# Performance work log

Measured on AMD Instinct MI355X. Metric: run time of the kernel, lower is better.

Reference implementation:

```python
import jax, jax.numpy as jnp
import numpy as np

N_NODES = 50000
N_EDGES = 800000
D = 64  # in_dim = hidden_dim = out_dim


def gcn_conv(x, edge_index, W, b, num_nodes):
    """PyG GCNConv: x' = D^{-1/2} (A + I) D^{-1/2} (x W) + b."""
    h = x @ W  # [N, out]
    # add self-loops
    loop = jnp.arange(num_nodes, dtype=edge_index.dtype)
    row = jnp.concatenate([edge_index[0], loop])  # sources j
    col = jnp.concatenate([edge_index[1], loop])  # targets i
    # symmetric normalization
    ones = jnp.ones(row.shape[0], dtype=h.dtype)
    deg = jax.ops.segment_sum(ones, col, num_segments=num_nodes)
    dinv = jnp.where(deg > 0, jax.lax.rsqrt(deg), 0.0)
    norm = dinv[row] * dinv[col]  # [E+N]
    # gather -> scale -> scatter-add
    msg = h[row] * norm[:, None]
    out = jax.ops.segment_sum(msg, col, num_segments=num_nodes)
    return out + b


def setup_inputs() -> dict:
    key = jax.random.key(0)
    k = jax.random.split(key, 6)
    x = jax.random.normal(k[0], (N_NODES, D), dtype=jnp.float32)
    edge_index = jax.random.randint(k[1], (2, N_EDGES), 0, N_NODES, dtype=jnp.int64)
    s = 1.0 / np.sqrt(D)
    W1 = jax.random.uniform(k[2], (D, D), jnp.float32, -s, s)
    b1 = jnp.zeros((D,), jnp.float32)
    W2 = jax.random.uniform(k[3], (D, D), jnp.float32, -s, s)
    b2 = jnp.zeros((D,), jnp.float32)
    return {"x": x, "edge_index": edge_index, "W1": W1, "b1": b1, "W2": W2, "b2": b2}


def reference(x, edge_index, W1, b1, W2, b2):
    h = gcn_conv(x, edge_index, W1, b1, N_NODES)
    h = jax.nn.relu(h)
    out = gcn_conv(h, edge_index, W2, b2, N_NODES)
    return out
```

## Files before the change

### kernel.cpp

```cpp
#include <hip/hip_runtime.h>
#include <hip/hip_fp16.h>

#define N_NODES 50000
#define N_EDGES 800000
#define D 64
#define RANGES 8
#define SLICES 16
#define NPB (N_NODES / RANGES)
#define I4S (N_EDGES / SLICES / 4)
#define CAP 48
#define PFX_BLOCKS (N_NODES / 4)
#define GEMM_BLOCKS (N_NODES / 16)

__global__ __launch_bounds__(1024)
void count_kernel(const int* __restrict__ col, unsigned char* __restrict__ cnt8) {
    __shared__ int cur[NPB];
    int tid = threadIdx.x;
    int r = blockIdx.x & (RANGES - 1), s = blockIdx.x >> 3;
    int lo = r * NPB;
    for (int i = tid; i < NPB; i += 1024) cur[i] = 0;
    __syncthreads();
    const int4* c4 = (const int4*)col;
    for (int i = s * I4S + tid; i < (s + 1) * I4S; i += 1024) {
        int4 c = c4[i];
        int dx = c.x - lo, dy = c.y - lo, dz = c.z - lo, dw = c.w - lo;
        if ((unsigned)dx < NPB) atomicAdd(&cur[dx], 1);
        if ((unsigned)dy < NPB) atomicAdd(&cur[dy], 1);
        if ((unsigned)dz < NPB) atomicAdd(&cur[dz], 1);
        if ((unsigned)dw < NPB) atomicAdd(&cur[dw], 1);
    }
    __syncthreads();
    for (int i = tid; i < NPB; i += 1024)
        cnt8[(size_t)s * N_NODES + lo + i] = (unsigned char)min(cur[i], 255);
}

__device__ __forceinline__ void gemm_body(int blk, const float* __restrict__ X,
                                          const float* __restrict__ W,
                                          __half* __restrict__ H) {
    int tid = threadIdx.x, lane = tid & 63, wv = tid >> 6;
    float w[64];
    #pragma unroll
    for (int k = 0; k < 64; ++k) w[k] = W[k * 64 + lane];
    int node0 = blk * 16 + wv * 4;
    #pragma unroll
    for (int r = 0; r < 4; ++r) {
        int node = node0 + r;
        float xv = X[node * 64 + lane];
        float a0 = 0.f, a1 = 0.f;
        #pragma unroll
        for (int k = 0; k < 64; k += 2) {
            a0 = fmaf(__shfl(xv, k, 64),     w[k],     a0);
            a1 = fmaf(__shfl(xv, k + 1, 64), w[k + 1], a1);
        }
        H[node * 64 + lane] = __float2half(a0 + a1);
    }
}

__global__ __launch_bounds__(256)
void prefix_gemm_kernel(const unsigned char* __restrict__ cnt8,
                        unsigned short* __restrict__ base16,
                        int* __restrict__ cntf, float* __restrict__ dinv,
                        const float* __restrict__ X, const float* __restrict__ W,
                        __half* __restrict__ H) {
    if (blockIdx.x < PFX_BLOCKS) {
        int tid = threadIdx.x, lane = tid & 63;
        int node = blockIdx.x * 4 + (tid >> 6);
        int c = 0;
        if (lane < SLICES) c = cnt8[(size_t)lane * N_NODES + node];
        int pin = c;
        #pragma unroll
        for (int off = 1; off < SLICES; off <<= 1) {
            int t = __shfl_up(pin, off, 64);
            if (lane >= off && lane < SLICES) pin += t;
        }
        if (lane < SLICES)
            base16[(size_t)lane * N_NODES + node] = (unsigned short)(pin - c);
        int n = __shfl(pin, SLICES - 1, 64);
        if (lane == 0) {
            cntf[node] = min(n, CAP);
            dinv[node] = rsqrtf((float)(n + 1));
        }
    } else {
        gemm_body(blockIdx.x - PFX_BLOCKS, X, W, H);
    }
}

__global__ __launch_bounds__(1024)
void place_kernel(const int* __restrict__ row, const int* __restrict__ col,
                  const unsigned short* __restrict__ base16,
                  unsigned short* __restrict__ srcs) {
    __shared__ int cur[NPB];
    int tid = threadIdx.x;
    int r = blockIdx.x & (RANGES - 1), s = blockIdx.x >> 3;
    int lo = r * NPB;
    for (int i = tid; i < NPB; i += 1024)
        cur[i] = base16[(size_t)s * N_NODES + lo + i];
    __syncthreads();
    const int4* c4 = (const int4*)col;
    const int4* r4 = (const int4*)row;
    for (int i = s * I4S + tid; i < (s + 1) * I4S; i += 1024) {
        int4 c  = c4[i];
        int4 rr = r4[i];
        int dx = c.x - lo, dy = c.y - lo, dz = c.z - lo, dw = c.w - lo;
        if ((unsigned)dx < NPB) {
            int p = atomicAdd(&cur[dx], 1);
            if (p < CAP) srcs[(size_t)(lo + dx) * CAP + p] = (unsigned short)rr.x;
        }
        if ((unsigned)dy < NPB) {
            int p = atomicAdd(&cur[dy], 1);
            if (p < CAP) srcs[(size_t)(lo + dy) * CAP + p] = (unsigned short)rr.y;
        }
        if ((unsigned)dz < NPB) {
            int p = atomicAdd(&cur[dz], 1);
            if (p < CAP) srcs[(size_t)(lo + dz) * CAP + p] = (unsigned short)rr.z;
        }
        if ((unsigned)dw < NPB) {
            int p = atomicAdd(&cur[dw], 1);
            if (p < CAP) srcs[(size_t)(lo + dw) * CAP + p] = (unsigned short)rr.w;
        }
    }
}

template<int FUSE>
__global__ __launch_bounds__(256)
void gather_kernel(const __half* __restrict__ H, const int* __restrict__ cnt,
                   const unsigned short* __restrict__ srcs,
                   const float* __restrict__ dinv,
                   const float* __restrict__ bias, const float* __restrict__ W2,
                   void* __restrict__ outp) {
    int tid = threadIdx.x, lane = tid & 63;
    int half = lane >> 5, sub = lane & 31;
    int node = blockIdx.x * 4 + (tid >> 6);
    int n = cnt[node];
    float di = dinv[node];
    const unsigned short* sp = srcs + (size_t)node * CAP;
    int e = 0;
    if (lane < n) {
        int s = sp[lane];
        float w = dinv[s];
        e = s | (((int)__half_as_ushort(__float2half(w))) << 16);
    }
    const __half2* H2 = (const __half2*)H;
    float2 self2 = __half22float2(H2[(size_t)node * 32 + sub]);
    float sw = (half == 0) ? di : 0.f;
    float ax = sw * self2.x, ay = sw * self2.y;
    int i0 = half;
    int nr = (n + 15) & ~15;
    for (int base = 0; base < nr; base += 16) {
        int b0 = base + i0;
        int q0 = __shfl(e, b0 + 0,  64), q1 = __shfl(e, b0 + 2,  64);
        int q2 = __shfl(e, b0 + 4,  64), q3 = __shfl(e, b0 + 6,  64);
        int q4 = __shfl(e, b0 + 8,  64), q5 = __shfl(e, b0 + 10, 64);
        int q6 = __shfl(e, b0 + 12, 64), q7 = __shfl(e, b0 + 14, 64);
        float2 v0 = __half22float2(H2[(size_t)(q0 & 0xFFFF) * 32 + sub]);
        float2 v1 = __half22float2(H2[(size_t)(q1 & 0xFFFF) * 32 + sub]);
        float2 v2 = __half22float2(H2[(size_t)(q2 & 0xFFFF) * 32 + sub]);
        float2 v3 = __half22float2(H2[(size_t)(q3 & 0xFFFF) * 32 + sub]);
        float2 v4 = __half22float2(H2[(size_t)(q4 & 0xFFFF) * 32 + sub]);
        float2 v5 = __half22float2(H2[(size_t)(q5 & 0xFFFF) * 32 + sub]);
        float2 v6 = __half22float2(H2[(size_t)(q6 & 0xFFFF) * 32 + sub]);
        float2 v7 = __half22float2(H2[(size_t)(q7 & 0xFFFF) * 32 + sub]);
        float w0 = __half2float(__ushort_as_half((unsigned short)((unsigned)q0 >> 16)));
        float w1 = __half2float(__ushort_as_half((unsigned short)((unsigned)q1 >> 16)));
        float w2 = __half2float(__ushort_as_half((unsigned short)((unsigned)q2 >> 16)));
        float w3 = __half2float(__ushort_as_half((unsigned short)((unsigned)q3 >> 16)));
        float w4 = __half2float(__ushort_as_half((unsigned short)((unsigned)q4 >> 16)));
        float w5 = __half2float(__ushort_as_half((unsigned short)((unsigned)q5 >> 16)));
        float w6 = __half2float(__ushort_as_half((unsigned short)((unsigned)q6 >> 16)));
        float w7 = __half2float(__ushort_as_half((unsigned short)((unsigned)q7 >> 16)));
        ax = fmaf(w0, v0.x, ax); ay = fmaf(w0, v0.y, ay);
        ax = fmaf(w1, v1.x, ax); ay = fmaf(w1, v1.y, ay);
        ax = fmaf(w2, v2.x, ax); ay = fmaf(w2, v2.y, ay);
        ax = fmaf(w3, v3.x, ax); ay = fmaf(w3, v3.y, ay);
        ax = fmaf(w4, v4.x, ax); ay = fmaf(w4, v4.y, ay);
        ax = fmaf(w5, v5.x, ax); ay = fmaf(w5, v5.y, ay);
        ax = fmaf(w6, v6.x, ax); ay = fmaf(w6, v6.y, ay);
        ax = fmaf(w7, v7.x, ax); ay = fmaf(w7, v7.y, ay);
    }
    ax += __shfl_xor(ax, 32, 64);
    ay += __shfl_xor(ay, 32, 64);
    float cx = __shfl(ax, lane >> 1, 64);
    float cy = __shfl(ay, lane >> 1, 64);
    float sum = (lane & 1) ? cy : cx;
    float gval = di * sum + bias[lane];
    if constexpr (FUSE) {
        gval = fmaxf(gval, 0.f);
        float wc[64];
        #pragma unroll
        for (int k = 0; k < 64; ++k) wc[k] = W2[k * 64 + lane];
        float o0 = 0.f, o1 = 0.f;
        #pragma unroll
        for (int k = 0; k < 64; k += 2) {
            o0 = fmaf(__shfl(gval, k, 64),     wc[k],     o0);
            o1 = fmaf(__shfl(gval, k + 1, 64), wc[k + 1], o1);
        }
        ((__half*)outp)[node * 64 + lane] = __float2half(o0 + o1);
    } else {
        ((float*)outp)[node * 64 + lane] = gval;
    }
}

extern "C" void kernel_launch(void* const* d_in, const int* in_sizes, int n_in,
                              void* d_out, int out_size, void* d_ws, size_t ws_size,
                              hipStream_t stream) {
    const float* x   = (const float*)d_in[0];
    const int*   ei  = (const int*)d_in[1];
    const int*   row = ei;
    const int*   col = ei + N_EDGES;
    const float* W1  = (const float*)d_in[2];
    const float* b1  = (const float*)d_in[3];
    const float* W2  = (const float*)d_in[4];
    const float* b2  = (const float*)d_in[5];
    float* out = (float*)d_out;

    char* p = (char*)d_ws;
    __half* h  = (__half*)p;           p += (size_t)N_NODES * D * 2;
    __half* h2 = (__half*)p;           p += (size_t)N_NODES * D * 2;
    unsigned char*  cnt8   = (unsigned char*)p;  p += (size_t)SLICES * N_NODES;
    unsigned short* base16 = (unsigned short*)p; p += (size_t)SLICES * N_NODES * 2;
    unsigned short* srcs   = (unsigned short*)p; p += (size_t)N_NODES * CAP * 2;
    float* dinv = (float*)p;           p += (size_t)N_NODES * 4;
    int*   cntf = (int*)p;             p += (size_t)N_NODES * 4;

    count_kernel<<<RANGES * SLICES, 1024, 0, stream>>>(col, cnt8);
    prefix_gemm_kernel<<<PFX_BLOCKS + GEMM_BLOCKS, 256, 0, stream>>>(
        cnt8, base16, cntf, dinv, x, W1, h);
    place_kernel<<<RANGES * SLICES, 1024, 0, stream>>>(row, col, base16, srcs);
    gather_kernel<1><<<N_NODES / 4, 256, 0, stream>>>(h, cntf, srcs, dinv, b1, W2, h2);
    gather_kernel<0><<<N_NODES / 4, 256, 0, stream>>>(h2, cntf, srcs, dinv, b2, nullptr, out);
}
```

Before: 214.0 us.

## Pack source weights into edge list, widen gather loads, split second GEMM

The place kernel now writes 32-bit packed entries holding the source index and its half-precision dinv, so the gather no longer does a dependent dinv lookup per edge. The gather is rebuilt so each group of 8 lanes loads a full 128-byte row as 16-byte vectors, processing 8 edges per step. The self-loop is appended as an extra edge entry, and results are reduced through shuffles and shared memory. The fused per-node W2 GEMM is moved out of the gather into a separate gemm2 kernel. This trades a larger edge buffer and one more launch for wider, fewer memory transactions and lower register pressure in the gather.

```diff
diff --git a/kernel.cpp b/kernel.cpp
--- a/kernel.cpp
+++ b/kernel.cpp
@@ -3,7 +3,6 @@
 
 #define N_NODES 50000
 #define N_EDGES 800000
-#define D 64
 #define RANGES 8
 #define SLICES 16
 #define NPB (N_NODES / RANGES)
@@ -34,7 +33,11 @@
         cnt8[(size_t)s * N_NODES + lo + i] = (unsigned char)min(cur[i], 255);
 }
 
-__device__ __forceinline__ void gemm_body(int blk, const float* __restrict__ X,
+__device__ __forceinline__ float ldf(float v)  { return v; }
+__device__ __forceinline__ float ldf(__half v) { return __half2float(v); }
+
+template<typename InT>
+__device__ __forceinline__ void gemm_body(int blk, const InT* __restrict__ X,
                                           const float* __restrict__ W,
                                           __half* __restrict__ H) {
     int tid = threadIdx.x, lane = tid & 63, wv = tid >> 6;
@@ -45,14 +48,14 @@
     #pragma unroll
     for (int r = 0; r < 4; ++r) {
         int node = node0 + r;
-        float xv = X[node * 64 + lane];
+        float xv = ldf(X[(size_t)node * 64 + lane]);
         float a0 = 0.f, a1 = 0.f;
         #pragma unroll
         for (int k = 0; k < 64; k += 2) {
             a0 = fmaf(__shfl(xv, k, 64),     w[k],     a0);
             a1 = fmaf(__shfl(xv, k + 1, 64), w[k + 1], a1);
         }
-        H[node * 64 + lane] = __float2half(a0 + a1);
+        H[(size_t)node * 64 + lane] = __float2half(a0 + a1);
     }
 }
 
@@ -60,6 +63,7 @@
 void prefix_gemm_kernel(const unsigned char* __restrict__ cnt8,
                         unsigned short* __restrict__ base16,
                         int* __restrict__ cntf, float* __restrict__ dinv,
+                        unsigned short* __restrict__ dinv16u,
                         const float* __restrict__ X, const float* __restrict__ W,
                         __half* __restrict__ H) {
     if (blockIdx.x < PFX_BLOCKS) {
@@ -77,8 +81,10 @@
             base16[(size_t)lane * N_NODES + node] = (unsigned short)(pin - c);
         int n = __shfl(pin, SLICES - 1, 64);
         if (lane == 0) {
+            float di = rsqrtf((float)(n + 1));
             cntf[node] = min(n, CAP);
-            dinv[node] = rsqrtf((float)(n + 1));
+            dinv[node] = di;
+            dinv16u[node] = __half_as_ushort(__float2half(di));
         }
     } else {
         gemm_body(blockIdx.x - PFX_BLOCKS, X, W, H);
@@ -88,7 +94,8 @@
 __global__ __launch_bounds__(1024)
 void place_kernel(const int* __restrict__ row, const int* __restrict__ col,
                   const unsigned short* __restrict__ base16,
-                  unsigned short* __restrict__ srcs) {
+                  const unsigned short* __restrict__ dinv16u,
+                  unsigned int* __restrict__ epk) {
     __shared__ int cur[NPB];
     int tid = threadIdx.x;
     int r = blockIdx.x & (RANGES - 1), s = blockIdx.x >> 3;
@@ -104,100 +111,97 @@
         int dx = c.x - lo, dy = c.y - lo, dz = c.z - lo, dw = c.w - lo;
         if ((unsigned)dx < NPB) {
             int p = atomicAdd(&cur[dx], 1);
-            if (p < CAP) srcs[(size_t)(lo + dx) * CAP + p] = (unsigned short)rr.x;
+            if (p < CAP) epk[(size_t)(lo + dx) * CAP + p]
+                = (unsigned)rr.x | ((unsigned)dinv16u[rr.x] << 16);
         }
         if ((unsigned)dy < NPB) {
             int p = atomicAdd(&cur[dy], 1);
-            if (p < CAP) srcs[(size_t)(lo + dy) * CAP + p] = (unsigned short)rr.y;
+            if (p < CAP) epk[(size_t)(lo + dy) * CAP + p]
+                = (unsigned)rr.y | ((unsigned)dinv16u[rr.y] << 16);
         }
         if ((unsigned)dz < NPB) {
             int p = atomicAdd(&cur[dz], 1);
-            if (p < CAP) srcs[(size_t)(lo + dz) * CAP + p] = (unsigned short)rr.z;
+            if (p < CAP) epk[(size_t)(lo + dz) * CAP + p]
+                = (unsigned)rr.z | ((unsigned)dinv16u[rr.z] << 16);
         }
         if ((unsigned)dw < NPB) {
             int p = atomicAdd(&cur[dw], 1);
-            if (p < CAP) srcs[(size_t)(lo + dw) * CAP + p] = (unsigned short)rr.w;
-        }
-    }
-}
-
-template<int FUSE>
+            if (p < CAP) epk[(size_t)(lo + dw) * CAP + p]
+                = (unsigned)rr.w | ((unsigned)dinv16u[rr.w] << 16);
+        }
+    }
+}
+
+template<int MODE>
 __global__ __launch_bounds__(256)
-void gather_kernel(const __half* __restrict__ H, const int* __restrict__ cnt,
-                   const unsigned short* __restrict__ srcs,
+void gather_kernel(const __half* __restrict__ H, const int* __restrict__ cntf,
+                   const unsigned int* __restrict__ epk,
                    const float* __restrict__ dinv,
-                   const float* __restrict__ bias, const float* __restrict__ W2,
-                   void* __restrict__ outp) {
-    int tid = threadIdx.x, lane = tid & 63;
-    int half = lane >> 5, sub = lane & 31;
-    int node = blockIdx.x * 4 + (tid >> 6);
-    int n = cnt[node];
+                   const float* __restrict__ bias, void* __restrict__ outp) {
+    __shared__ float xg[4][64];
+    int tid = threadIdx.x, lane = tid & 63, wv = tid >> 6;
+    int node = blockIdx.x * 4 + wv;
+    int n = cntf[node];
     float di = dinv[node];
-    const unsigned short* sp = srcs + (size_t)node * CAP;
-    int e = 0;
-    if (lane < n) {
-        int s = sp[lane];
-        float w = dinv[s];
-        e = s | (((int)__half_as_ushort(__float2half(w))) << 16);
-    }
-    const __half2* H2 = (const __half2*)H;
-    float2 self2 = __half22float2(H2[(size_t)node * 32 + sub]);
-    float sw = (half == 0) ? di : 0.f;
-    float ax = sw * self2.x, ay = sw * self2.y;
-    int i0 = half;
-    int nr = (n + 15) & ~15;
-    for (int base = 0; base < nr; base += 16) {
-        int b0 = base + i0;
-        int q0 = __shfl(e, b0 + 0,  64), q1 = __shfl(e, b0 + 2,  64);
-        int q2 = __shfl(e, b0 + 4,  64), q3 = __shfl(e, b0 + 6,  64);
-        int q4 = __shfl(e, b0 + 8,  64), q5 = __shfl(e, b0 + 10, 64);
-        int q6 = __shfl(e, b0 + 12, 64), q7 = __shfl(e, b0 + 14, 64);
-        float2 v0 = __half22float2(H2[(size_t)(q0 & 0xFFFF) * 32 + sub]);
-        float2 v1 = __half22float2(H2[(size_t)(q1 & 0xFFFF) * 32 + sub]);
-        float2 v2 = __half22float2(H2[(size_t)(q2 & 0xFFFF) * 32 + sub]);
-        float2 v3 = __half22float2(H2[(size_t)(q3 & 0xFFFF) * 32 + sub]);
-        float2 v4 = __half22float2(H2[(size_t)(q4 & 0xFFFF) * 32 + sub]);
-        float2 v5 = __half22float2(H2[(size_t)(q5 & 0xFFFF) * 32 + sub]);
-        float2 v6 = __half22float2(H2[(size_t)(q6 & 0xFFFF) * 32 + sub]);
-        float2 v7 = __half22float2(H2[(size_t)(q7 & 0xFFFF) * 32 + sub]);
-        float w0 = __half2float(__ushort_as_half((unsigned short)((unsigned)q0 >> 16)));
-        float w1 = __half2float(__ushort_as_half((unsigned short)((unsigned)q1 >> 16)));
-        float w2 = __half2float(__ushort_as_half((unsigned short)((unsigned)q2 >> 16)));
-        float w3 = __half2float(__ushort_as_half((unsigned short)((unsigned)q3 >> 16)));
-        float w4 = __half2float(__ushort_as_half((unsigned short)((unsigned)q4 >> 16)));
-        float w5 = __half2float(__ushort_as_half((unsigned short)((unsigned)q5 >> 16)));
-        float w6 = __half2float(__ushort_as_half((unsigned short)((unsigned)q6 >> 16)));
-        float w7 = __half2float(__ushort_as_half((unsigned short)((unsigned)q7 >> 16)));
-        ax = fmaf(w0, v0.x, ax); ay = fmaf(w0, v0.y, ay);
-        ax = fmaf(w1, v1.x, ax); ay = fmaf(w1, v1.y, ay);
-        ax = fmaf(w2, v2.x, ax); ay = fmaf(w2, v2.y, ay);
-        ax = fmaf(w3, v3.x, ax); ay = fmaf(w3, v3.y, ay);
-        ax = fmaf(w4, v4.x, ax); ay = fmaf(w4, v4.y, ay);
-        ax = fmaf(w5, v5.x, ax); ay = fmaf(w5, v5.y, ay);
-        ax = fmaf(w6, v6.x, ax); ay = fmaf(w6, v6.y, ay);
-        ax = fmaf(w7, v7.x, ax); ay = fmaf(w7, v7.y, ay);
-    }
-    ax += __shfl_xor(ax, 32, 64);
-    ay += __shfl_xor(ay, 32, 64);
-    float cx = __shfl(ax, lane >> 1, 64);
-    float cy = __shfl(ay, lane >> 1, 64);
-    float sum = (lane & 1) ? cy : cx;
-    float gval = di * sum + bias[lane];
-    if constexpr (FUSE) {
-        gval = fmaxf(gval, 0.f);
-        float wc[64];
-        #pragma unroll
-        for (int k = 0; k < 64; ++k) wc[k] = W2[k * 64 + lane];
-        float o0 = 0.f, o1 = 0.f;
-        #pragma unroll
-        for (int k = 0; k < 64; k += 2) {
-            o0 = fmaf(__shfl(gval, k, 64),     wc[k],     o0);
-            o1 = fmaf(__shfl(gval, k + 1, 64), wc[k + 1], o1);
-        }
-        ((__half*)outp)[node * 64 + lane] = __float2half(o0 + o1);
+    unsigned int e = 0;
+    if (lane < n) e = epk[(size_t)node * CAP + lane];
+    if (lane == n)
+        e = (unsigned)node
+          | ((unsigned)__half_as_ushort(__float2half(di)) << 16);
+    int m = n + 1;
+    int grp = lane >> 3, off = lane & 7;
+    const float4* H4 = (const float4*)H;
+    float a0=0.f,a1=0.f,a2=0.f,a3=0.f,a4=0.f,a5=0.f,a6=0.f,a7=0.f;
+    int nr = (m + 15) & ~15;
+    for (int j = 0; j < nr; j += 16) {
+        unsigned qa = (unsigned)__shfl((int)e, j + grp, 64);
+        unsigned qb = (unsigned)__shfl((int)e, j + 8 + grp, 64);
+        float4 va = H4[(size_t)(qa & 0xFFFFu) * 8 + off];
+        float4 vb = H4[(size_t)(qb & 0xFFFFu) * 8 + off];
+        float wa = __half2float(__ushort_as_half((unsigned short)(qa >> 16)));
+        float wb = __half2float(__ushort_as_half((unsigned short)(qb >> 16)));
+        const __half2* ha = (const __half2*)&va;
+        float2 f0 = __half22float2(ha[0]), f1 = __half22float2(ha[1]);
+        float2 f2 = __half22float2(ha[2]), f3 = __half22float2(ha[3]);
+        a0 = fmaf(wa, f0.x, a0); a1 = fmaf(wa, f0.y, a1);
+        a2 = fmaf(wa, f1.x, a2); a3 = fmaf(wa, f1.y, a3);
+        a4 = fmaf(wa, f2.x, a4); a5 = fmaf(wa, f2.y, a5);
+        a6 = fmaf(wa, f3.x, a6); a7 = fmaf(wa, f3.y, a7);
+        const __half2* hb = (const __half2*)&vb;
+        f0 = __half22float2(hb[0]); f1 = __half22float2(hb[1]);
+        f2 = __half22float2(hb[2]); f3 = __half22float2(hb[3]);
+        a0 = fmaf(wb, f0.x, a0); a1 = fmaf(wb, f0.y, a1);
+        a2 = fmaf(wb, f1.x, a2); a3 = fmaf(wb, f1.y, a3);
+        a4 = fmaf(wb, f2.x, a4); a5 = fmaf(wb, f2.y, a5);
+        a6 = fmaf(wb, f3.x, a6); a7 = fmaf(wb, f3.y, a7);
+    }
+    a0 += __shfl_xor(a0, 8, 64); a0 += __shfl_xor(a0, 16, 64); a0 += __shfl_xor(a0, 32, 64);
+    a1 += __shfl_xor(a1, 8, 64); a1 += __shfl_xor(a1, 16, 64); a1 += __shfl_xor(a1, 32, 64);
+    a2 += __shfl_xor(a2, 8, 64); a2 += __shfl_xor(a2, 16, 64); a2 += __shfl_xor(a2, 32, 64);
+    a3 += __shfl_xor(a3, 8, 64); a3 += __shfl_xor(a3, 16, 64); a3 += __shfl_xor(a3, 32, 64);
+    a4 += __shfl_xor(a4, 8, 64); a4 += __shfl_xor(a4, 16, 64); a4 += __shfl_xor(a4, 32, 64);
+    a5 += __shfl_xor(a5, 8, 64); a5 += __shfl_xor(a5, 16, 64); a5 += __shfl_xor(a5, 32, 64);
+    a6 += __shfl_xor(a6, 8, 64); a6 += __shfl_xor(a6, 16, 64); a6 += __shfl_xor(a6, 32, 64);
+    a7 += __shfl_xor(a7, 8, 64); a7 += __shfl_xor(a7, 16, 64); a7 += __shfl_xor(a7, 32, 64);
+    if (lane < 8) {
+        xg[wv][lane * 8 + 0] = a0; xg[wv][lane * 8 + 1] = a1;
+        xg[wv][lane * 8 + 2] = a2; xg[wv][lane * 8 + 3] = a3;
+        xg[wv][lane * 8 + 4] = a4; xg[wv][lane * 8 + 5] = a5;
+        xg[wv][lane * 8 + 6] = a6; xg[wv][lane * 8 + 7] = a7;
+    }
+    float sum = xg[wv][lane];
+    float res = di * sum + bias[lane];
+    if constexpr (MODE == 0) {
+        ((__half*)outp)[(size_t)node * 64 + lane] = __float2half(fmaxf(res, 0.f));
     } else {
-        ((float*)outp)[node * 64 + lane] = gval;
-    }
+        ((float*)outp)[(size_t)node * 64 + lane] = res;
+    }
+}
+
+__global__ __launch_bounds__(256)
+void gemm2_kernel(const __half* __restrict__ G, const float* __restrict__ W,
+                  __half* __restrict__ H) {
+    gemm_body(blockIdx.x, G, W, H);
 }
 
 extern "C" void kernel_launch(void* const* d_in, const int* in_sizes, int n_in,
@@ -214,18 +218,20 @@
     float* out = (float*)d_out;
 
     char* p = (char*)d_ws;
-    __half* h  = (__half*)p;           p += (size_t)N_NODES * D * 2;
-    __half* h2 = (__half*)p;           p += (size_t)N_NODES * D * 2;
-    unsigned char*  cnt8   = (unsigned char*)p;  p += (size_t)SLICES * N_NODES;
-    unsigned short* base16 = (unsigned short*)p; p += (size_t)SLICES * N_NODES * 2;
-    unsigned short* srcs   = (unsigned short*)p; p += (size_t)N_NODES * CAP * 2;
-    float* dinv = (float*)p;           p += (size_t)N_NODES * 4;
-    int*   cntf = (int*)p;             p += (size_t)N_NODES * 4;
+    __half* h  = (__half*)p;            p += (size_t)N_NODES * 64 * 2;
+    __half* g  = (__half*)p;            p += (size_t)N_NODES * 64 * 2;
+    unsigned char*  cnt8    = (unsigned char*)p;  p += (size_t)SLICES * N_NODES;
+    unsigned short* base16  = (unsigned short*)p; p += (size_t)SLICES * N_NODES * 2;
+    unsigned int*   epk     = (unsigned int*)p;   p += (size_t)N_NODES * CAP * 4;
+    float*          dinv    = (float*)p;          p += (size_t)N_NODES * 4;
+    unsigned short* dinv16u = (unsigned short*)p; p += (size_t)N_NODES * 2;
+    int*            cntf    = (int*)p;            p += (size_t)N_NODES * 4;
 
     count_kernel<<<RANGES * SLICES, 1024, 0, stream>>>(col, cnt8);
     prefix_gemm_kernel<<<PFX_BLOCKS + GEMM_BLOCKS, 256, 0, stream>>>(
-        cnt8, base16, cntf, dinv, x, W1, h);
-    place_kernel<<<RANGES * SLICES, 1024, 0, stream>>>(row, col, base16, srcs);
-    gather_kernel<1><<<N_NODES / 4, 256, 0, stream>>>(h, cntf, srcs, dinv, b1, W2, h2);
-    gather_kernel<0><<<N_NODES / 4, 256, 0, stream>>>(h2, cntf, srcs, dinv, b2, nullptr, out);
-}
+        cnt8, base16, cntf, dinv, dinv16u, x, W1, h);
+    place_kernel<<<RANGES * SLICES, 1024, 0, stream>>>(row, col, base16, dinv16u, epk);
+    gather_kernel<0><<<N_NODES / 4, 256, 0, stream>>>(h, cntf, epk, dinv, b1, g);
+    gemm2_kernel<<<GEMM_BLOCKS, 256, 0, stream>>>(g, W2, h);
+    gather_kernel<1><<<N_NODES / 4, 256, 0, stream>>>(h, cntf, epk, dinv, b2, out);
+}
```

Result: slower. 241.9 us (+13.0%).
